# Kernel tuning notes

Hardware: AMD Instinct MI355X
Metric: run time of the kernel (lower is better)

The kernel has to match this reference:

```python
import jax, jax.numpy as jnp
import numpy as np

B, N, IN_DIM, HID = 8, 2048, 128, 64
LN_EPS = 1e-5
NEG_INF = -9e15
LRELU_SLOPE = 0.2


def setup_inputs() -> dict:
    key = jax.random.key(0)
    k1, k2, k3, k4, k5, k6 = jax.random.split(key, 6)
    stdv = 1.0 / np.sqrt(HID)
    adj = jax.random.randint(k1, (B, N, N), 0, 2, dtype=jnp.int32)
    # ensure self-loops so every row has at least one valid entry
    adj = adj.at[:, jnp.arange(N), jnp.arange(N)].set(1)
    return {
        "adj": adj,
        "x": jax.random.normal(k2, (B, N, IN_DIM), dtype=jnp.float32),
        "h": jax.random.normal(k3, (B, N, HID), dtype=jnp.float32),
        "X2H": jax.random.uniform(k4, (IN_DIM, 3 * HID), minval=-stdv, maxval=stdv, dtype=jnp.float32),
        "H2H": jax.random.uniform(k5, (HID, 3 * HID), minval=-stdv, maxval=stdv, dtype=jnp.float32),
        "a": jax.random.uniform(k6, (2 * HID, 1), minval=-stdv, maxval=stdv, dtype=jnp.float32),
    }


def _gated_inputs(x, h, X2H, H2H):
    gate_x = x @ X2H          # [B,N,3H]
    gate_h = h @ H2H          # [B,N,3H]
    i_r, i_i, i_n = jnp.split(gate_x, 3, axis=2)
    h_r, h_i, h_n = jnp.split(gate_h, 3, axis=2)
    resetgate = jax.nn.sigmoid(i_r + h_r)
    inputgate = jax.nn.sigmoid(i_i + h_i)
    irh = i_n + resetgate * h_n
    mu = jnp.mean(irh, axis=-1, keepdims=True)
    var = jnp.mean(jnp.square(irh - mu), axis=-1, keepdims=True)
    irh = (irh - mu) * jax.lax.rsqrt(var + LN_EPS)  # layer_norm, no affine
    newgate = jnp.tanh(irh)
    return newgate + inputgate * (h - newgate)


def reference(adj, x, h, X2H, H2H, a):
    Wh = _gated_inputs(x, h, X2H, H2H)              # [B,N,H]
    Wh1 = Wh @ a[:HID]                              # [B,N,1]
    Wh2 = Wh @ a[HID:]                              # [B,N,1]
    e = jax.nn.leaky_relu(Wh1 + jnp.swapaxes(Wh2, 1, 2), LRELU_SLOPE)  # [B,N,N]
    scores = jnp.where(adj != 0, e, jnp.float32(NEG_INF))
    attention = jax.nn.softmax(scores, axis=2)
    h_prime = attention @ Wh                        # [B,N,H]
    return (h_prime, Wh)
```

## Files before the change

### kernel.cpp

```cpp
#include <hip/hip_runtime.h>

constexpr int BB  = 8;
constexpr int NN  = 2048;
constexpr int IND = 128;
constexpr int HD  = 64;
constexpr float LN_EPS = 1e-5f;
constexpr float SLOPE  = 0.2f;

typedef _Float16 half8 __attribute__((ext_vector_type(8)));
typedef float    f32x4 __attribute__((ext_vector_type(4)));

__device__ __forceinline__ float wave_sum(float v) {
    #pragma unroll
    for (int off = 32; off > 0; off >>= 1) v += __shfl_xor(v, off);
    return v;
}
__device__ __forceinline__ float wave_max(float v) {
    #pragma unroll
    for (int off = 32; off > 0; off >>= 1) v = fmaxf(v, __shfl_xor(v, off));
    return v;
}

__global__ __launch_bounds__(256) void k_gates(
    const float* __restrict__ x, const float* __restrict__ h,
    const float* __restrict__ X2H, const float* __restrict__ H2H,
    const float* __restrict__ a,
    float* __restrict__ Wh_out, _Float16* __restrict__ Whh,
    float* __restrict__ Wh1, float* __restrict__ Wh2)
{
    const int lane = threadIdx.x & 63;
    const int wid  = threadIdx.x >> 6;
    const int base = (blockIdx.x * 4 + wid) * 8;

    float gx0[8] = {0}, gx1[8] = {0}, gx2[8] = {0};
    float gh0[8] = {0}, gh1[8] = {0}, gh2[8] = {0};

    for (int d4 = 0; d4 < IND; d4 += 4) {
        float w0[4], w1[4], w2[4];
        #pragma unroll
        for (int dd = 0; dd < 4; ++dd) {
            const float* wp = X2H + (size_t)(d4 + dd) * 192;
            w0[dd] = wp[lane]; w1[dd] = wp[64 + lane]; w2[dd] = wp[128 + lane];
        }
        #pragma unroll
        for (int rr = 0; rr < 8; ++rr) {
            f32x4 xv = *(const f32x4*)(x + (size_t)(base + rr) * IND + d4);
            #pragma unroll
            for (int dd = 0; dd < 4; ++dd) {
                gx0[rr] = fmaf(xv[dd], w0[dd], gx0[rr]);
                gx1[rr] = fmaf(xv[dd], w1[dd], gx1[rr]);
                gx2[rr] = fmaf(xv[dd], w2[dd], gx2[rr]);
            }
        }
    }
    for (int d4 = 0; d4 < HD; d4 += 4) {
        float w0[4], w1[4], w2[4];
        #pragma unroll
        for (int dd = 0; dd < 4; ++dd) {
            const float* wp = H2H + (size_t)(d4 + dd) * 192;
            w0[dd] = wp[lane]; w1[dd] = wp[64 + lane]; w2[dd] = wp[128 + lane];
        }
        #pragma unroll
        for (int rr = 0; rr < 8; ++rr) {
            f32x4 hv = *(const f32x4*)(h + (size_t)(base + rr) * HD + d4);
            #pragma unroll
            for (int dd = 0; dd < 4; ++dd) {
                gh0[rr] = fmaf(hv[dd], w0[dd], gh0[rr]);
                gh1[rr] = fmaf(hv[dd], w1[dd], gh1[rr]);
                gh2[rr] = fmaf(hv[dd], w2[dd], gh2[rr]);
            }
        }
    }

    const float a0 = a[lane], a1 = a[64 + lane];
    for (int rr = 0; rr < 8; ++rr) {
        const int row = base + rr;
        const float hr = h[(size_t)row * HD + lane];
        const float rg = 1.f / (1.f + __expf(-(gx0[rr] + gh0[rr])));
        const float ig = 1.f / (1.f + __expf(-(gx1[rr] + gh1[rr])));
        float irh = gx2[rr] + rg * gh2[rr];
        const float mu = wave_sum(irh) * (1.f / 64.f);
        const float dv = irh - mu;
        const float var = wave_sum(dv * dv) * (1.f / 64.f);
        const float ng = tanhf(dv * rsqrtf(var + LN_EPS));
        const float wh = ng + ig * (hr - ng);
        Wh_out[(size_t)row * HD + lane] = wh;
        Whh[(size_t)row * HD + lane] = (_Float16)wh;
        const float d1 = wave_sum(wh * a0);
        const float d2 = wave_sum(wh * a1);
        if (lane == 0) { Wh1[row] = d1; Wh2[row] = d2; }
    }
}

constexpr int PSTR = NN + 8;

__global__ __launch_bounds__(256) void k_attn(
    const int* __restrict__ adj,
    const _Float16* __restrict__ Whh,
    const float* __restrict__ Wh1, const float* __restrict__ Wh2,
    float* __restrict__ hp)
{
    __shared__ float Wh2s[NN];
    __shared__ __align__(16) _Float16 Pbuf[16 * PSTR];
    __shared__ float redbuf[4];
    __shared__ float lsum[16];
    __shared__ float wh1s[16];

    const int tid  = threadIdx.x;
    const int lane = tid & 63;
    const int wid  = tid >> 6;
    const int b    = blockIdx.x >> 7;
    const int i0   = (blockIdx.x & 127) * 16;

    for (int j = tid; j < NN; j += 256) Wh2s[j] = Wh2[b * NN + j];
    if (tid < 16) wh1s[tid] = Wh1[b * NN + i0 + tid];
    __syncthreads();

    for (int r = 0; r < 16; ++r) {
        const int row = i0 + r;
        const float w1 = wh1s[r];
        const int* __restrict__ arow = adj + ((size_t)b * NN + row) * NN;

        float s[8];
        float mx = -3e38f;
        #pragma unroll
        for (int k = 0; k < 8; ++k) {
            const int j = tid + k * 256;
            const int av = arow[j];
            const float t = w1 + Wh2s[j];
            const float e = (t > 0.f) ? t : SLOPE * t;
            s[k] = av ? e : -1e30f;
            mx = fmaxf(mx, s[k]);
        }
        mx = wave_max(mx);
        __syncthreads();
        if (lane == 0) redbuf[wid] = mx;
        __syncthreads();
        mx = fmaxf(fmaxf(redbuf[0], redbuf[1]), fmaxf(redbuf[2], redbuf[3]));

        float sum = 0.f;
        #pragma unroll
        for (int k = 0; k < 8; ++k) {
            const int j = tid + k * 256;
            const float p = __expf(s[k] - mx);
            sum += p;
            Pbuf[r * PSTR + j] = (_Float16)p;
        }
        sum = wave_sum(sum);
        __syncthreads();
        if (lane == 0) redbuf[wid] = sum;
        __syncthreads();
        if (tid == 0) lsum[r] = redbuf[0] + redbuf[1] + redbuf[2] + redbuf[3];
    }
    __syncthreads();

    const int n0 = wid * 16;
    const int m  = lane & 15;
    const int q  = lane >> 4;
    const _Float16* __restrict__ Wb = Whh + (size_t)b * NN * HD;

    f32x4 acc = {0.f, 0.f, 0.f, 0.f};
    for (int k0 = 0; k0 < NN; k0 += 32) {
        const int kq = k0 + q * 8;
        const half8 av = *(const half8*)(&Pbuf[m * PSTR + kq]);
        half8 bv;
        #pragma unroll
        for (int jj = 0; jj < 8; ++jj)
            bv[jj] = Wb[(size_t)(kq + jj) * HD + n0 + m];
        acc = __builtin_amdgcn_mfma_f32_16x16x32_f16(av, bv, acc, 0, 0, 0);
    }
    #pragma unroll
    for (int r2 = 0; r2 < 4; ++r2) {
        const int irow = q * 4 + r2;
        const float inv = 1.f / lsum[irow];
        hp[((size_t)b * NN + i0 + irow) * HD + n0 + m] = acc[r2] * inv;
    }
}

extern "C" void kernel_launch(void* const* d_in, const int* in_sizes, int n_in,
                              void* d_out, int out_size, void* d_ws, size_t ws_size,
                              hipStream_t stream) {
    const int*   adj = (const int*)d_in[0];
    const float* x   = (const float*)d_in[1];
    const float* h   = (const float*)d_in[2];
    const float* X2H = (const float*)d_in[3];
    const float* H2H = (const float*)d_in[4];
    const float* a   = (const float*)d_in[5];

    float* out = (float*)d_out;
    float* hp  = out;
    float* Wh  = out + (size_t)BB * NN * HD;

    float*    Wh1 = (float*)d_ws;
    float*    Wh2 = Wh1 + BB * NN;
    _Float16* Whh = (_Float16*)(Wh2 + BB * NN);

    k_gates<<<dim3((BB * NN) / 32), dim3(256), 0, stream>>>(
        x, h, X2H, H2H, a, Wh, Whh, Wh1, Wh2);
    k_attn<<<dim3(BB * (NN / 16)), dim3(256), 0, stream>>>(
        adj, Whh, Wh1, Wh2, hp);
}
```

Baseline: 272.6 us.

## Use analytic softmax max bound, wave-per-row scoring, and MFMA-packed fp16 Wh layout

Replaces the per-row masked max reduction with a per-batch bound: leaky_relu is monotonic, so leaky_relu(Wh1_i + max Wh2) upper-bounds every score in the row. This removes four block-wide barriers per row, and each wave now handles four rows using vectorized int4 adj loads. k_gates writes the fp16 Wh copy in a k-packed half8 layout, so the MFMA B operand is a single 16-byte load instead of eight strided scalar loads. The risk is that the bound can exceed the true masked max by a lot, which could underflow the fp16 probabilities or reduce accuracy.

```diff
diff --git a/kernel.cpp b/kernel.cpp
--- a/kernel.cpp
+++ b/kernel.cpp
@@ -8,6 +8,7 @@
 constexpr float SLOPE  = 0.2f;
 
 typedef _Float16 half8 __attribute__((ext_vector_type(8)));
+typedef _Float16 half4 __attribute__((ext_vector_type(4)));
 typedef float    f32x4 __attribute__((ext_vector_type(4)));
 
 __device__ __forceinline__ float wave_sum(float v) {
@@ -25,7 +26,7 @@
     const float* __restrict__ x, const float* __restrict__ h,
     const float* __restrict__ X2H, const float* __restrict__ H2H,
     const float* __restrict__ a,
-    float* __restrict__ Wh_out, _Float16* __restrict__ Whh,
+    float* __restrict__ Wh_out, _Float16* __restrict__ Whh2,
     float* __restrict__ Wh1, float* __restrict__ Wh2)
 {
     const int lane = threadIdx.x & 63;
@@ -73,6 +74,7 @@
     }
 
     const float a0 = a[lane], a1 = a[64 + lane];
+    half8 p8;
     for (int rr = 0; rr < 8; ++rr) {
         const int row = base + rr;
         const float hr = h[(size_t)row * HD + lane];
@@ -85,26 +87,25 @@
         const float ng = tanhf(dv * rsqrtf(var + LN_EPS));
         const float wh = ng + ig * (hr - ng);
         Wh_out[(size_t)row * HD + lane] = wh;
-        Whh[(size_t)row * HD + lane] = (_Float16)wh;
+        p8[rr] = (_Float16)wh;
         const float d1 = wave_sum(wh * a0);
         const float d2 = wave_sum(wh * a1);
         if (lane == 0) { Wh1[row] = d1; Wh2[row] = d2; }
     }
+    *(half8*)(Whh2 + ((size_t)(base >> 3) * 64 + lane) * 8) = p8;
 }
 
 constexpr int PSTR = NN + 8;
 
 __global__ __launch_bounds__(256) void k_attn(
     const int* __restrict__ adj,
-    const _Float16* __restrict__ Whh,
+    const _Float16* __restrict__ Whh2,
     const float* __restrict__ Wh1, const float* __restrict__ Wh2,
     float* __restrict__ hp)
 {
-    __shared__ float Wh2s[NN];
     __shared__ __align__(16) _Float16 Pbuf[16 * PSTR];
     __shared__ float redbuf[4];
     __shared__ float lsum[16];
-    __shared__ float wh1s[16];
 
     const int tid  = threadIdx.x;
     const int lane = tid & 63;
@@ -112,61 +113,64 @@
     const int b    = blockIdx.x >> 7;
     const int i0   = (blockIdx.x & 127) * 16;
 
-    for (int j = tid; j < NN; j += 256) Wh2s[j] = Wh2[b * NN + j];
-    if (tid < 16) wh1s[tid] = Wh1[b * NN + i0 + tid];
+    f32x4 wv[8];
+    const f32x4* __restrict__ w2v = (const f32x4*)(Wh2 + (size_t)b * NN);
+    #pragma unroll
+    for (int k = 0; k < 8; ++k) wv[k] = w2v[lane + 64 * k];
+
+    float mx = -3e38f;
+    #pragma unroll
+    for (int k = 0; k < 8; ++k)
+        mx = fmaxf(mx, fmaxf(fmaxf(wv[k][0], wv[k][1]), fmaxf(wv[k][2], wv[k][3])));
+    mx = wave_max(mx);
+    if (lane == 0) redbuf[wid] = mx;
     __syncthreads();
-
-    for (int r = 0; r < 16; ++r) {
-        const int row = i0 + r;
-        const float w1 = wh1s[r];
-        const int* __restrict__ arow = adj + ((size_t)b * NN + row) * NN;
-
-        float s[8];
-        float mx = -3e38f;
+    const float M = fmaxf(fmaxf(redbuf[0], redbuf[1]), fmaxf(redbuf[2], redbuf[3]));
+
+    const int4* __restrict__ atile = (const int4*)(adj + ((size_t)b * NN + i0) * NN);
+    #pragma unroll
+    for (int rr = 0; rr < 4; ++rr) {
+        const int r = wid * 4 + rr;
+        const float w1 = Wh1[b * NN + i0 + r];
+        const float t0 = w1 + M;
+        const float c  = (t0 > 0.f) ? t0 : SLOPE * t0;
+        const int4* __restrict__ arow = atile + (size_t)r * (NN / 4);
+
+        int4 av[8];
+        #pragma unroll
+        for (int k = 0; k < 8; ++k) av[k] = arow[lane + 64 * k];
+
+        float sum = 0.f;
         #pragma unroll
         for (int k = 0; k < 8; ++k) {
-            const int j = tid + k * 256;
-            const int av = arow[j];
-            const float t = w1 + Wh2s[j];
-            const float e = (t > 0.f) ? t : SLOPE * t;
-            s[k] = av ? e : -1e30f;
-            mx = fmaxf(mx, s[k]);
-        }
-        mx = wave_max(mx);
-        __syncthreads();
-        if (lane == 0) redbuf[wid] = mx;
-        __syncthreads();
-        mx = fmaxf(fmaxf(redbuf[0], redbuf[1]), fmaxf(redbuf[2], redbuf[3]));
-
-        float sum = 0.f;
-        #pragma unroll
-        for (int k = 0; k < 8; ++k) {
-            const int j = tid + k * 256;
-            const float p = __expf(s[k] - mx);
-            sum += p;
-            Pbuf[r * PSTR + j] = (_Float16)p;
+            const int ai[4] = {av[k].x, av[k].y, av[k].z, av[k].w};
+            half4 ph;
+            #pragma unroll
+            for (int d = 0; d < 4; ++d) {
+                const float t = w1 + wv[k][d];
+                const float e = (t > 0.f) ? t : SLOPE * t;
+                const float p = ai[d] ? __expf(e - c) : 0.f;
+                sum += p;
+                ph[d] = (_Float16)p;
+            }
+            *(half4*)&Pbuf[r * PSTR + 4 * (lane + 64 * k)] = ph;
         }
         sum = wave_sum(sum);
-        __syncthreads();
-        if (lane == 0) redbuf[wid] = sum;
-        __syncthreads();
-        if (tid == 0) lsum[r] = redbuf[0] + redbuf[1] + redbuf[2] + redbuf[3];
+        if (lane == 0) lsum[r] = sum;
     }
     __syncthreads();
 
     const int n0 = wid * 16;
     const int m  = lane & 15;
     const int q  = lane >> 4;
-    const _Float16* __restrict__ Wb = Whh + (size_t)b * NN * HD;
+    const half8* __restrict__ Wp = (const half8*)(Whh2 + (size_t)b * NN * HD);
+    const _Float16* __restrict__ prow = &Pbuf[m * PSTR];
 
     f32x4 acc = {0.f, 0.f, 0.f, 0.f};
+    #pragma unroll 4
     for (int k0 = 0; k0 < NN; k0 += 32) {
-        const int kq = k0 + q * 8;
-        const half8 av = *(const half8*)(&Pbuf[m * PSTR + kq]);
-        half8 bv;
-        #pragma unroll
-        for (int jj = 0; jj < 8; ++jj)
-            bv[jj] = Wb[(size_t)(kq + jj) * HD + n0 + m];
+        const half8 av = *(const half8*)(prow + k0 + q * 8);
+        const half8 bv = Wp[((k0 >> 3) + q) * 64 + n0 + m];
         acc = __builtin_amdgcn_mfma_f32_16x16x32_f16(av, bv, acc, 0, 0, 0);
     }
     #pragma unroll
@@ -191,12 +195,12 @@
     float* hp  = out;
     float* Wh  = out + (size_t)BB * NN * HD;
 
-    float*    Wh1 = (float*)d_ws;
-    float*    Wh2 = Wh1 + BB * NN;
-    _Float16* Whh = (_Float16*)(Wh2 + BB * NN);
+    float*    Wh1  = (float*)d_ws;
+    float*    Wh2  = Wh1 + BB * NN;
+    _Float16* Whh2 = (_Float16*)(Wh2 + BB * NN);
 
     k_gates<<<dim3((BB * NN) / 32), dim3(256), 0, stream>>>(
-        x, h, X2H, H2H, a, Wh, Whh, Wh1, Wh2);
+        x, h, X2H, H2H, a, Wh, Whh2, Wh1, Wh2);
     k_attn<<<dim3(BB * (NN / 16)), dim3(256), 0, stream>>>(
-        adj, Whh, Wh1, Wh2, hp);
-}
+        adj, Whh2, Wh1, Wh2, hp);
+}
```

Measured after the change: 259.0 us. 1.05x faster.
